# Optimization experiments

Measured on AMD Instinct MI355X. Metric: run time of the kernel, lower is better.

Reference implementation:

```python
import jax, jax.numpy as jnp
import numpy as np

N, L, C, KF = 32, 1024, 3, 256
H = C * KF            # hidden_dim = 768
M = 3072              # mlp_dim
EPS = 1e-6


def setup_inputs() -> dict:
    key = jax.random.key(0)
    ks = jax.random.split(key, 14)
    s = lambda fan: 1.0 / np.sqrt(fan)
    return {
        "x": jax.random.normal(ks[0], (N, L, H), dtype=jnp.float32),
        # per-channel QKV linears: Linear(k_factor, 3*k_factor) for each channel
        "W_qkv": jax.random.normal(ks[1], (C, KF, 3 * KF), dtype=jnp.float32) * s(KF),
        "b_qkv": jax.random.normal(ks[2], (C, 3 * KF), dtype=jnp.float32) * 0.01,
        "W_out": jax.random.normal(ks[3], (KF, KF), dtype=jnp.float32) * s(KF),
        "b_out": jax.random.normal(ks[4], (KF,), dtype=jnp.float32) * 0.01,
        "ln1_g": jnp.ones((H,), jnp.float32),
        "ln1_b": jnp.zeros((H,), jnp.float32),
        "ln2_g": jnp.ones((H,), jnp.float32),
        "ln2_b": jnp.zeros((H,), jnp.float32),
        "W1": jax.random.normal(ks[5], (H, M), dtype=jnp.float32) * s(H),
        "b1": jax.random.normal(ks[6], (M,), dtype=jnp.float32) * 1e-6,
        "W2": jax.random.normal(ks[7], (M, H), dtype=jnp.float32) * s(M),
        "b2": jax.random.normal(ks[8], (H,), dtype=jnp.float32) * 1e-6,
    }


def _ln(x, g, b):
    mu = jnp.mean(x, axis=-1, keepdims=True)
    var = jnp.mean(jnp.square(x - mu), axis=-1, keepdims=True)
    return (x - mu) * jax.lax.rsqrt(var + EPS) * g + b


def _criss_cross_attn(h, W_qkv, b_qkv, W_out, b_out):
    # h: [N, L, H]; hidden layout is channel-major: (C, KF)
    hc = h.reshape(h.shape[0], h.shape[1], C, KF)
    qkv = jnp.einsum("nlck,ckd->nlcd", hc, W_qkv) + b_qkv      # [N,L,C,3KF]
    q, k, v = jnp.split(qkv, 3, axis=-1)                        # each [N,L,C,KF]
    # move k_factor axis before channel axis: [N,L,KF,C]
    q = jnp.swapaxes(q, -1, -2)
    k = jnp.swapaxes(k, -1, -2)
    v = jnp.swapaxes(v, -1, -2)
    # outer-product scores over channels: [N,L,KF,C,C]
    scores = q[..., :, None] * k[..., None, :] / np.sqrt(KF)
    attn = jax.nn.softmax(scores, axis=-1)
    # einsum 'ijklm,ijkl->ijkm': sum over first channel axis
    ctx = jnp.einsum("nlkcd,nlkc->nlkd", attn, v)               # [N,L,KF,C]
    ctx = jnp.swapaxes(ctx, -1, -2)                             # [N,L,C,KF]
    out = ctx @ W_out + b_out                                   # fc_out per k_factor
    return out.reshape(h.shape[0], h.shape[1], H)


def reference(x, W_qkv, b_qkv, W_out, b_out, ln1_g, ln1_b, ln2_g, ln2_b, W1, b1, W2, b2):
    h = _ln(x, ln1_g, ln1_b)
    a = _criss_cross_attn(h, W_qkv, b_qkv, W_out, b_out)
    xr = a + x                                                   # residual (dropout=0)
    y = _ln(xr, ln2_g, ln2_b)
    y = jax.nn.gelu(y @ W1 + b1, approximate=False) @ W2 + b2    # MLPBlock
    return xr + y
```

## Files before the change

kernel.cpp:

```cpp
#include <hip/hip_runtime.h>
#include <hip/hip_bf16.h>
#include <math.h>

#define CDIV(a,b) (((a)+(b)-1)/(b))

typedef __attribute__((ext_vector_type(8))) short short8;
typedef __attribute__((ext_vector_type(4))) float f32x4;

__device__ __forceinline__ float bf2f(__hip_bfloat16 h) { return __bfloat162float(h); }
__device__ __forceinline__ __hip_bfloat16 f2bf(float f) { return __float2bfloat16(f); }

__device__ __forceinline__ float gelu_f(float v) {
  const float u = v * (0.7978845608f + 0.0356774081f * v * v);
  const float e = __expf(2.0f * u);
  const float t = 1.0f - 2.0f * __builtin_amdgcn_rcpf(e + 1.0f);
  return 0.5f * v * (1.0f + t);
}

__global__ __launch_bounds__(256) void ln_kernel(
    const float* __restrict__ in, const float* __restrict__ g,
    const float* __restrict__ b, __hip_bfloat16* __restrict__ out)
{
  __shared__ float sm1[4], sm2[4];
  const int row = blockIdx.x;
  const int tid = threadIdx.x;
  const float* p = in + (size_t)row * 768;
  float x0 = p[tid], x1 = p[tid + 256], x2 = p[tid + 512];
  float s = x0 + x1 + x2;
  #pragma unroll
  for (int off = 32; off > 0; off >>= 1) s += __shfl_down(s, off, 64);
  const int l = tid & 63, w = tid >> 6;
  if (l == 0) sm1[w] = s;
  __syncthreads();
  const float mu = (sm1[0] + sm1[1] + sm1[2] + sm1[3]) * (1.0f / 768.0f);
  const float d0 = x0 - mu, d1 = x1 - mu, d2 = x2 - mu;
  float ss = d0*d0 + d1*d1 + d2*d2;
  #pragma unroll
  for (int off = 32; off > 0; off >>= 1) ss += __shfl_down(ss, off, 64);
  if (l == 0) sm2[w] = ss;
  __syncthreads();
  const float var = (sm2[0] + sm2[1] + sm2[2] + sm2[3]) * (1.0f / 768.0f);
  const float rstd = rsqrtf(var + 1e-6f);
  __hip_bfloat16* q = out + (size_t)row * 768;
  q[tid]       = f2bf(d0 * rstd * g[tid]       + b[tid]);
  q[tid + 256] = f2bf(d1 * rstd * g[tid + 256] + b[tid + 256]);
  q[tid + 512] = f2bf(d2 * rstd * g[tid + 512] + b[tid + 512]);
}

__global__ __launch_bounds__(256) void attn_kernel(
    const __hip_bfloat16* __restrict__ qkv, __hip_bfloat16* __restrict__ ctx)
{
  const long t = (long)blockIdx.x * 256 + threadIdx.x;
  const long row = t >> 8;
  const int kf = (int)(t & 255);
  const __hip_bfloat16* p = qkv + row * 2304;
  float q[3], k[3], v[3];
  #pragma unroll
  for (int c = 0; c < 3; ++c) {
    q[c] = bf2f(p[c*768 + kf]);
    k[c] = bf2f(p[c*768 + 256 + kf]);
    v[c] = bf2f(p[c*768 + 512 + kf]);
  }
  float o0 = 0.f, o1 = 0.f, o2 = 0.f;
  #pragma unroll
  for (int c = 0; c < 3; ++c) {
    const float s0 = q[c]*k[0]*0.0625f, s1 = q[c]*k[1]*0.0625f, s2 = q[c]*k[2]*0.0625f;
    const float m = fmaxf(s0, fmaxf(s1, s2));
    const float e0 = __expf(s0-m), e1 = __expf(s1-m), e2 = __expf(s2-m);
    const float inv = v[c] / (e0 + e1 + e2);
    o0 += e0*inv; o1 += e1*inv; o2 += e2*inv;
  }
  __hip_bfloat16* o = ctx + row * 768;
  o[kf] = f2bf(o0); o[256+kf] = f2bf(o1); o[512+kf] = f2bf(o2);
}

__global__ __launch_bounds__(256) void transpose_bf16_kernel(
    const float* __restrict__ in, __hip_bfloat16* __restrict__ out, int K, int N)
{
  in  += (size_t)blockIdx.y * K * N;
  out += (size_t)blockIdx.y * K * N;
  const int t = blockIdx.x * 256 + threadIdx.x;
  if (t >= K * N) return;
  const int k = t / N, n = t - k * N;
  out[(size_t)n * K + k] = f2bf(in[t]);
}

#define BM 128
#define BN 128
#define BK 64

template<int MODE>
__global__ __launch_bounds__(256) void gemm_bt_kernel(
    const __hip_bfloat16* __restrict__ A, int lda, long strideA,
    const __hip_bfloat16* __restrict__ Bt, int ldb, long strideB,
    float* __restrict__ Cf, __hip_bfloat16* __restrict__ Cb, int ldc, long strideC,
    const float* __restrict__ bias, long strideBias,
    const float* __restrict__ res,
    int K)
{
  __shared__ __align__(16) __hip_bfloat16 sA[BM * BK];
  __shared__ __align__(16) __hip_bfloat16 sB[BN * BK];

  const int z = blockIdx.z;
  A    += (size_t)z * strideA;
  Bt   += (size_t)z * strideB;
  bias += (size_t)z * strideBias;
  const long cOff = (long)z * strideC;

  const int  tileN = blockIdx.x * BN;
  const long tileM = (long)blockIdx.y * BM;

  const int tid  = threadIdx.x;
  const int lane = tid & 63;
  const int wv   = tid >> 6;
  const int waveM = (wv & 1) * 64;
  const int waveN = (wv >> 1) * 64;

  const int srow  = tid >> 3;
  const int selem = ((tid & 7) ^ (srow & 7)) * 8;
  const int frow = lane & 15;
  const int fswz = (lane & 7) << 4;
  const int fkb  = (lane >> 4) << 4;

  f32x4 acc[4][4] = {};

  char* const sAb = (char*)sA;
  char* const sBb = (char*)sB;

  for (int k0 = 0; k0 < K; k0 += BK) {
    #pragma unroll
    for (int hh = 0; hh < 4; ++hh) {
      const int r = hh * 32 + srow;
      const __hip_bfloat16* ga = A  + (tileM + r) * (size_t)lda + k0 + selem;
      const __hip_bfloat16* gb = Bt + ((long)tileN + r) * (size_t)ldb + k0 + selem;
      __builtin_amdgcn_global_load_lds(
          (const __attribute__((address_space(1))) void*)ga,
          (__attribute__((address_space(3))) void*)(sAb + hh*4096 + tid*16),
          16, 0, 0);
      __builtin_amdgcn_global_load_lds(
          (const __attribute__((address_space(1))) void*)gb,
          (__attribute__((address_space(3))) void*)(sBb + hh*4096 + tid*16),
          16, 0, 0);
    }
    __syncthreads();

    #pragma unroll
    for (int s = 0; s < 2; ++s) {
      const int kb = fkb + s * 64;
      short8 aF[4], bF[4];
      #pragma unroll
      for (int i = 0; i < 4; ++i)
        aF[i] = *(const short8*)(sAb + (waveM + i*16 + frow) * 128 + (kb ^ fswz));
      #pragma unroll
      for (int j = 0; j < 4; ++j)
        bF[j] = *(const short8*)(sBb + (waveN + j*16 + frow) * 128 + (kb ^ fswz));
      #pragma unroll
      for (int i = 0; i < 4; ++i)
        #pragma unroll
        for (int j = 0; j < 4; ++j)
          acc[i][j] = __builtin_amdgcn_mfma_f32_16x16x32_bf16(aF[i], bF[j], acc[i][j], 0, 0, 0);
    }
    __syncthreads();
  }

  #pragma unroll
  for (int i = 0; i < 4; ++i) {
    const long row0 = tileM + waveM + i*16 + ((lane >> 4) * 4);
    #pragma unroll
    for (int j = 0; j < 4; ++j) {
      const int col = tileN + waveN + j*16 + (lane & 15);
      const float bv = bias[col];
      #pragma unroll
      for (int r = 0; r < 4; ++r) {
        const long idx = cOff + (row0 + r) * (long)ldc + col;
        const float v = acc[i][j][r] + bv;
        if (MODE == 0) {
          Cb[idx] = f2bf(v);
        } else if (MODE == 1 || MODE == 3) {
          Cf[idx] = v + res[idx];
        } else {
          Cb[idx] = f2bf(gelu_f(v));
        }
      }
    }
  }
}

extern "C" void kernel_launch(void* const* d_in, const int* in_sizes, int n_in,
                              void* d_out, int out_size, void* d_ws, size_t ws_size,
                              hipStream_t stream)
{
  const float* x     = (const float*)d_in[0];
  const float* W_qkv = (const float*)d_in[1];
  const float* b_qkv = (const float*)d_in[2];
  const float* W_out = (const float*)d_in[3];
  const float* b_out = (const float*)d_in[4];
  const float* ln1_g = (const float*)d_in[5];
  const float* ln1_b = (const float*)d_in[6];
  const float* ln2_g = (const float*)d_in[7];
  const float* ln2_b = (const float*)d_in[8];
  const float* W1    = (const float*)d_in[9];
  const float* b1    = (const float*)d_in[10];
  const float* W2    = (const float*)d_in[11];
  const float* b2    = (const float*)d_in[12];
  float* out = (float*)d_out;

  char* ws = (char*)d_ws;
  __hip_bfloat16* h     = (__hip_bfloat16*)(ws + 0);
  __hip_bfloat16* qkv   = (__hip_bfloat16*)(ws + 50331648);
  __hip_bfloat16* ctx   = (__hip_bfloat16*)(ws + 0);
  __hip_bfloat16* act   = (__hip_bfloat16*)(ws + 0);
  __hip_bfloat16* yln   = (__hip_bfloat16*)(ws + 201326592);
  __hip_bfloat16* wqkvT = (__hip_bfloat16*)(ws + 251658240);
  __hip_bfloat16* woutT = (__hip_bfloat16*)(ws + 252837888);
  __hip_bfloat16* w1T   = (__hip_bfloat16*)(ws + 252968960);
  __hip_bfloat16* w2T   = (__hip_bfloat16*)(ws + 257687552);

  transpose_bf16_kernel<<<dim3(CDIV(256*768,256), 3), 256, 0, stream>>>(W_qkv, wqkvT, 256, 768);
  transpose_bf16_kernel<<<dim3(CDIV(256*256,256), 1), 256, 0, stream>>>(W_out, woutT, 256, 256);
  transpose_bf16_kernel<<<dim3(CDIV(768*3072,256),1), 256, 0, stream>>>(W1, w1T, 768, 3072);
  transpose_bf16_kernel<<<dim3(CDIV(3072*768,256),1), 256, 0, stream>>>(W2, w2T, 3072, 768);

  ln_kernel<<<32768, 256, 0, stream>>>(x, ln1_g, ln1_b, h);

  gemm_bt_kernel<0><<<dim3(768/BN, 32768/BM, 3), 256, 0, stream>>>(
      h, 768, 256, wqkvT, 256, 768*256, nullptr, qkv, 2304, 768, b_qkv, 768, nullptr, 256);

  attn_kernel<<<32768, 256, 0, stream>>>(qkv, ctx);

  gemm_bt_kernel<1><<<dim3(256/BN, 98304/BM, 1), 256, 0, stream>>>(
      ctx, 256, 0, woutT, 256, 0, out, nullptr, 256, 0, b_out, 0, x, 256);

  ln_kernel<<<32768, 256, 0, stream>>>(out, ln2_g, ln2_b, yln);

  gemm_bt_kernel<2><<<dim3(3072/BN, 32768/BM, 1), 256, 0, stream>>>(
      yln, 768, 0, w1T, 768, 0, nullptr, act, 3072, 0, b1, 0, nullptr, 768);

  gemm_bt_kernel<3><<<dim3(768/BN, 32768/BM, 1), 256, 0, stream>>>(
      act, 3072, 0, w2T, 3072, 0, out, nullptr, 768, 0, b2, 0, out, 3072);
}
```

Measured before the change: 953.5 us.

## Halve GEMM K-tile, swap grid order, vectorize attention, tile weight transposes

The GEMM K-tile drops from 64 to 32, with the LDS swizzle reworked to match, which halves shared memory per block to allow more resident blocks. The grid is reordered so M tiles run along blockIdx.x, making consecutive blocks share the same weight tile. The attention kernel now processes two k_factor elements per thread using bf16x2 loads and stores, and the weight transposes use a 32x32 shared-memory tile to coalesce writes. The smaller K-tile doubles the barriers per unit of K work and shortens each stretch of MFMA work between loads.

```diff
diff --git a/kernel.cpp b/kernel.cpp
--- a/kernel.cpp
+++ b/kernel.cpp
@@ -48,46 +48,61 @@
 }
 
 __global__ __launch_bounds__(256) void attn_kernel(
-    const __hip_bfloat16* __restrict__ qkv, __hip_bfloat16* __restrict__ ctx)
+    const __hip_bfloat162* __restrict__ qkv, __hip_bfloat162* __restrict__ ctx)
 {
   const long t = (long)blockIdx.x * 256 + threadIdx.x;
-  const long row = t >> 8;
-  const int kf = (int)(t & 255);
-  const __hip_bfloat16* p = qkv + row * 2304;
-  float q[3], k[3], v[3];
+  const long row = t >> 7;
+  const int kp = (int)(t & 127);
+  const __hip_bfloat162* p = qkv + row * 1152;
+  float q[3][2], k[3][2], v[3][2];
   #pragma unroll
   for (int c = 0; c < 3; ++c) {
-    q[c] = bf2f(p[c*768 + kf]);
-    k[c] = bf2f(p[c*768 + 256 + kf]);
-    v[c] = bf2f(p[c*768 + 512 + kf]);
-  }
-  float o0 = 0.f, o1 = 0.f, o2 = 0.f;
-  #pragma unroll
-  for (int c = 0; c < 3; ++c) {
-    const float s0 = q[c]*k[0]*0.0625f, s1 = q[c]*k[1]*0.0625f, s2 = q[c]*k[2]*0.0625f;
-    const float m = fmaxf(s0, fmaxf(s1, s2));
-    const float e0 = __expf(s0-m), e1 = __expf(s1-m), e2 = __expf(s2-m);
-    const float inv = v[c] / (e0 + e1 + e2);
-    o0 += e0*inv; o1 += e1*inv; o2 += e2*inv;
-  }
-  __hip_bfloat16* o = ctx + row * 768;
-  o[kf] = f2bf(o0); o[256+kf] = f2bf(o1); o[512+kf] = f2bf(o2);
+    __hip_bfloat162 qq = p[c*384 + kp];
+    __hip_bfloat162 kk = p[c*384 + 128 + kp];
+    __hip_bfloat162 vv = p[c*384 + 256 + kp];
+    q[c][0] = __low2float(qq); q[c][1] = __high2float(qq);
+    k[c][0] = __low2float(kk); k[c][1] = __high2float(kk);
+    v[c][0] = __low2float(vv); v[c][1] = __high2float(vv);
+  }
+  float o[3][2] = {};
+  #pragma unroll
+  for (int u = 0; u < 2; ++u) {
+    #pragma unroll
+    for (int c = 0; c < 3; ++c) {
+      const float s0 = q[c][u]*k[0][u]*0.0625f, s1 = q[c][u]*k[1][u]*0.0625f, s2 = q[c][u]*k[2][u]*0.0625f;
+      const float m = fmaxf(s0, fmaxf(s1, s2));
+      const float e0 = __expf(s0-m), e1 = __expf(s1-m), e2 = __expf(s2-m);
+      const float inv = v[c][u] / (e0 + e1 + e2);
+      o[0][u] += e0*inv; o[1][u] += e1*inv; o[2][u] += e2*inv;
+    }
+  }
+  __hip_bfloat162* po = ctx + row * 384;
+  #pragma unroll
+  for (int d = 0; d < 3; ++d)
+    po[d*128 + kp] = __hip_bfloat162{f2bf(o[d][0]), f2bf(o[d][1])};
 }
 
 __global__ __launch_bounds__(256) void transpose_bf16_kernel(
     const float* __restrict__ in, __hip_bfloat16* __restrict__ out, int K, int N)
 {
-  in  += (size_t)blockIdx.y * K * N;
-  out += (size_t)blockIdx.y * K * N;
-  const int t = blockIdx.x * 256 + threadIdx.x;
-  if (t >= K * N) return;
-  const int k = t / N, n = t - k * N;
-  out[(size_t)n * K + k] = f2bf(in[t]);
+  __shared__ float tile[32][33];
+  in  += (size_t)blockIdx.z * K * N;
+  out += (size_t)blockIdx.z * K * N;
+  const int n0 = blockIdx.x * 32;
+  const int k0 = blockIdx.y * 32;
+  const int tx = threadIdx.x & 31, ty = threadIdx.x >> 5;
+  #pragma unroll
+  for (int r = 0; r < 32; r += 8)
+    tile[ty + r][tx] = in[(size_t)(k0 + ty + r) * N + n0 + tx];
+  __syncthreads();
+  #pragma unroll
+  for (int r = 0; r < 32; r += 8)
+    out[(size_t)(n0 + ty + r) * K + k0 + tx] = f2bf(tile[tx][ty + r]);
 }
 
 #define BM 128
 #define BN 128
-#define BK 64
+#define BK 32
 
 template<int MODE>
 __global__ __launch_bounds__(256) void gemm_bt_kernel(
@@ -107,8 +122,8 @@
   bias += (size_t)z * strideBias;
   const long cOff = (long)z * strideC;
 
-  const int  tileN = blockIdx.x * BN;
-  const long tileM = (long)blockIdx.y * BM;
+  const long tileM = (long)blockIdx.x * BM;
+  const int  tileN = blockIdx.y * BN;
 
   const int tid  = threadIdx.x;
   const int lane = tid & 63;
@@ -116,11 +131,11 @@
   const int waveM = (wv & 1) * 64;
   const int waveN = (wv >> 1) * 64;
 
-  const int srow  = tid >> 3;
-  const int selem = ((tid & 7) ^ (srow & 7)) * 8;
+  const int srow  = tid >> 2;
+  const int selem = ((tid & 3) ^ (srow & 3)) * 8;
   const int frow = lane & 15;
-  const int fswz = (lane & 7) << 4;
-  const int fkb  = (lane >> 4) << 4;
+  const int fq16 = (lane >> 4) << 4;
+  const int fkb  = (fq16 ^ ((frow & 3) << 4));
 
   f32x4 acc[4][4] = {};
 
@@ -129,8 +144,8 @@
 
   for (int k0 = 0; k0 < K; k0 += BK) {
     #pragma unroll
-    for (int hh = 0; hh < 4; ++hh) {
-      const int r = hh * 32 + srow;
+    for (int hh = 0; hh < 2; ++hh) {
+      const int r = hh * 64 + srow;
       const __hip_bfloat16* ga = A  + (tileM + r) * (size_t)lda + k0 + selem;
       const __hip_bfloat16* gb = Bt + ((long)tileN + r) * (size_t)ldb + k0 + selem;
       __builtin_amdgcn_global_load_lds(
@@ -144,22 +159,18 @@
     }
     __syncthreads();
 
-    #pragma unroll
-    for (int s = 0; s < 2; ++s) {
-      const int kb = fkb + s * 64;
-      short8 aF[4], bF[4];
-      #pragma unroll
-      for (int i = 0; i < 4; ++i)
-        aF[i] = *(const short8*)(sAb + (waveM + i*16 + frow) * 128 + (kb ^ fswz));
+    short8 aF[4], bF[4];
+    #pragma unroll
+    for (int i = 0; i < 4; ++i)
+      aF[i] = *(const short8*)(sAb + (waveM + i*16 + frow) * 64 + fkb);
+    #pragma unroll
+    for (int j = 0; j < 4; ++j)
+      bF[j] = *(const short8*)(sBb + (waveN + j*16 + frow) * 64 + fkb);
+    #pragma unroll
+    for (int i = 0; i < 4; ++i)
       #pragma unroll
       for (int j = 0; j < 4; ++j)
-        bF[j] = *(const short8*)(sBb + (waveN + j*16 + frow) * 128 + (kb ^ fswz));
-      #pragma unroll
-      for (int i = 0; i < 4; ++i)
-        #pragma unroll
-        for (int j = 0; j < 4; ++j)
-          acc[i][j] = __builtin_amdgcn_mfma_f32_16x16x32_bf16(aF[i], bF[j], acc[i][j], 0, 0, 0);
-    }
+        acc[i][j] = __builtin_amdgcn_mfma_f32_16x16x32_bf16(aF[i], bF[j], acc[i][j], 0, 0, 0);
     __syncthreads();
   }
 
@@ -216,26 +227,26 @@
   __hip_bfloat16* w1T   = (__hip_bfloat16*)(ws + 252968960);
   __hip_bfloat16* w2T   = (__hip_bfloat16*)(ws + 257687552);
 
-  transpose_bf16_kernel<<<dim3(CDIV(256*768,256), 3), 256, 0, stream>>>(W_qkv, wqkvT, 256, 768);
-  transpose_bf16_kernel<<<dim3(CDIV(256*256,256), 1), 256, 0, stream>>>(W_out, woutT, 256, 256);
-  transpose_bf16_kernel<<<dim3(CDIV(768*3072,256),1), 256, 0, stream>>>(W1, w1T, 768, 3072);
-  transpose_bf16_kernel<<<dim3(CDIV(3072*768,256),1), 256, 0, stream>>>(W2, w2T, 3072, 768);
+  transpose_bf16_kernel<<<dim3(768/32, 256/32, 3), 256, 0, stream>>>(W_qkv, wqkvT, 256, 768);
+  transpose_bf16_kernel<<<dim3(256/32, 256/32, 1), 256, 0, stream>>>(W_out, woutT, 256, 256);
+  transpose_bf16_kernel<<<dim3(3072/32, 768/32, 1), 256, 0, stream>>>(W1, w1T, 768, 3072);
+  transpose_bf16_kernel<<<dim3(768/32, 3072/32, 1), 256, 0, stream>>>(W2, w2T, 3072, 768);
 
   ln_kernel<<<32768, 256, 0, stream>>>(x, ln1_g, ln1_b, h);
 
-  gemm_bt_kernel<0><<<dim3(768/BN, 32768/BM, 3), 256, 0, stream>>>(
+  gemm_bt_kernel<0><<<dim3(32768/BM, 768/BN, 3), 256, 0, stream>>>(
       h, 768, 256, wqkvT, 256, 768*256, nullptr, qkv, 2304, 768, b_qkv, 768, nullptr, 256);
 
-  attn_kernel<<<32768, 256, 0, stream>>>(qkv, ctx);
-
-  gemm_bt_kernel<1><<<dim3(256/BN, 98304/BM, 1), 256, 0, stream>>>(
+  attn_kernel<<<16384, 256, 0, stream>>>((const __hip_bfloat162*)qkv, (__hip_bfloat162*)ctx);
+
+  gemm_bt_kernel<1><<<dim3(98304/BM, 256/BN, 1), 256, 0, stream>>>(
       ctx, 256, 0, woutT, 256, 0, out, nullptr, 256, 0, b_out, 0, x, 256);
 
   ln_kernel<<<32768, 256, 0, stream>>>(out, ln2_g, ln2_b, yln);
 
-  gemm_bt_kernel<2><<<dim3(3072/BN, 32768/BM, 1), 256, 0, stream>>>(
+  gemm_bt_kernel<2><<<dim3(32768/BM, 3072/BN, 1), 256, 0, stream>>>(
       yln, 768, 0, w1T, 768, 0, nullptr, act, 3072, 0, b1, 0, nullptr, 768);
 
-  gemm_bt_kernel<3><<<dim3(768/BN, 32768/BM, 1), 256, 0, stream>>>(
+  gemm_bt_kernel<3><<<dim3(32768/BM, 768/BN, 1), 256, 0, stream>>>(
       act, 3072, 0, w2T, 3072, 0, out, nullptr, 768, 0, b2, 0, out, 3072);
 }
```

Result: no change. 971.0 us (+1.8%).
